# Optimization experiments

Hardware: AMD Instinct MI355X
Metric: run time of the kernel (lower is better)

The kernel has to match this reference:

```python
import jax, jax.numpy as jnp
import numpy as np

B, L, D, DK, DV = 8, 2048, 1024, 1024, 1024

def setup_inputs() -> dict:
    key = jax.random.key(0)
    ks = jax.random.split(key, 8)
    # scale inputs/weights down so exp(scores) is numerically stable
    # (original softmax has no max-subtraction)
    x = jax.random.normal(ks[0], (B, L, D), dtype=jnp.float32) * 0.05
    Wq = jax.random.normal(ks[1], (D, DK), dtype=jnp.float32) * 0.05
    bq = jax.random.normal(ks[2], (DK,), dtype=jnp.float32) * 0.05
    Wk = jax.random.normal(ks[3], (D, DK), dtype=jnp.float32) * 0.05
    bk = jax.random.normal(ks[4], (DK,), dtype=jnp.float32) * 0.05
    Wv = jax.random.normal(ks[5], (D, DV), dtype=jnp.float32) * 0.05
    bv = jax.random.normal(ks[6], (DV,), dtype=jnp.float32) * 0.05
    actulength = jax.random.randint(ks[7], (B,), 1, L, dtype=jnp.int32)
    return {"x": x, "actulength": actulength, "Wq": Wq, "bq": bq,
            "Wk": Wk, "bk": bk, "Wv": Wv, "bv": bv}

def reference(x, actulength, Wq, bq, Wk, bk, Wv, bv):
    # QKV projections
    Q = x @ Wq + bq                      # [B, L, DK]
    K = x @ Wk + bk                      # [B, L, DK]
    V = x @ Wv + bv                      # [B, L, DV]
    scale = 1.0 / jnp.sqrt(jnp.float32(DK))
    scores = jnp.einsum('bld,bmd->blm', Q, K) * scale  # [B, L, L]
    # custom padding-aware softmax: subtract padding count from the sum
    s = jnp.exp(scores)
    tsum = jnp.sum(s, axis=2)            # [B, L]
    padding = (L - actulength).astype(s.dtype)[:, None]  # [B, 1]
    atten = s / (tsum - padding)[:, :, None]
    return jnp.einsum('blm,bmv->blv', atten, V)  # [B, L, DV]
```

## Files before the change

### kernel.cpp

```cpp
#include <hip/hip_runtime.h>
#include <hip/hip_bf16.h>
#include <cstdint>

#define DEV __device__ __forceinline__

typedef __attribute__((ext_vector_type(8))) __bf16 bf16x8;
typedef __attribute__((ext_vector_type(4))) float f32x4;

DEV ushort f2bf(float f){
  uint32_t u = __builtin_bit_cast(uint32_t, f);
  u += 0x7fffu + ((u >> 16) & 1u);
  return (ushort)(u >> 16);
}

DEV void gll16(const void* g, void* l){
  __builtin_amdgcn_global_load_lds((const __attribute__((address_space(1))) void*)g,
                                   (__attribute__((address_space(3))) void*)l, 16, 0, 0);
}

template<int MODE>
__global__ __launch_bounds__(512, 2) void gemm256(
    const ushort* __restrict__ A, const ushort* __restrict__ Bt,
    const float* __restrict__ bias,
    ushort* __restrict__ Cb, float* __restrict__ Cf, ushort* __restrict__ VTout,
    int gm, int gn, int K, int lda, int ldb, int ldc,
    size_t sA, size_t sB, size_t sC,
    float scale, float* __restrict__ partial, const float* __restrict__ denom,
    int Mrows, int nch)
{
  __shared__ __align__(16) ushort As[4][128][64];
  __shared__ __align__(16) ushort Bs[4][128][64];

  const int tid  = threadIdx.x;
  const int lane = tid & 63, wid = tid >> 6;
  const int wm = wid >> 2, wn = wid & 3;
  const int lr = lane & 15, fq = lane >> 4;
  const int lrh = lr >> 1;
  const int lo2 = ((lane & 1) << 2) | fq;

  const int nwg = gridDim.x;
  const int per = nwg >> 3;
  const int id  = blockIdx.x;
  const int swz = (id & 7) * per + (id >> 3);
  const int gmn = gm * gn;
  const int bz  = swz / gmn;
  const int rr  = swz - bz * gmn;
  const int q4  = rr >> 4, w4 = rr & 15;
  const int nsm = gm >> 2;
  const int stm = q4 % nsm, stn = q4 / nsm;
  const int bm  = (stm << 2) + (w4 & 3);
  const int bn  = (stn << 2) + (w4 >> 2);

  const ushort* Ab = A  + (size_t)bz * sA + (size_t)bm * 256 * (size_t)lda;
  const ushort* Bb = Bt + (size_t)bz * sB + (size_t)bn * 256 * (size_t)ldb;
  const int NT = K >> 5;

  auto srcOff = [&](int c, int ld)->size_t{
    int R = c >> 3, ci = c & 7, u = ci ^ (R & 7);
    return (size_t)(2*R + (u >> 2)) * (size_t)(ld*2) + (size_t)((u & 3) << 4);
  };
  const char* srcA0 = (const char*)Ab + srcOff(tid,       lda);
  const char* srcA1 = (const char*)Ab + srcOff(512 + tid, lda);
  const char* srcB0 = (const char*)Bb + srcOff(tid,       ldb);
  const char* srcB1 = (const char*)Bb + srcOff(512 + tid, ldb);
  char* AsB = (char*)As;
  char* BsB = (char*)Bs;
  const int dst0 = (wid << 6) * 16;
  const int dst1 = (512 + (wid << 6)) * 16;

  auto stageA = [&](int t){
    const int sb = (t & 3) << 14;
    const size_t kb = (size_t)t << 6;
    gll16(srcA0 + kb, AsB + sb + dst0);
    gll16(srcA1 + kb, AsB + sb + dst1);
  };
  auto stageB = [&](int t){
    const int sb = (t & 3) << 14;
    const size_t kb = (size_t)t << 6;
    gll16(srcB0 + kb, BsB + sb + dst0);
    gll16(srcB1 + kb, BsB + sb + dst1);
  };

  f32x4 acc[8][4];
  const f32x4 z = {0.f, 0.f, 0.f, 0.f};
#pragma unroll
  for (int m = 0; m < 8; ++m)
#pragma unroll
    for (int n = 0; n < 4; ++n) acc[m][n] = z;

  const int cio  = (lo2 ^ lrh) << 3;
  const int aoff = (wm*64 + lrh)*64 + cio;
  const int boff = (wn*32 + lrh)*64 + cio;

  stageA(0); stageB(0); stageA(1); stageB(1);
  asm volatile("s_waitcnt vmcnt(4)" ::: "memory");
  __builtin_amdgcn_s_barrier();

  for (int t = 0; t < NT; ++t){
    const int s = t & 3;
    const ushort* Asl = (const ushort*)As + (size_t)s*8192;
    const ushort* Bsl = (const ushort*)Bs + (size_t)s*8192;
    const bool pre = (t + 2 < NT);

    bf16x8 bfv[4], af0[4];
#pragma unroll
    for (int n = 0; n < 4; ++n)
      bfv[n] = *(const bf16x8*)&Bsl[boff + n*512];
#pragma unroll
    for (int m = 0; m < 4; ++m)
      af0[m] = *(const bf16x8*)&Asl[aoff + m*512];
    if (pre) stageA(t + 2);
    __builtin_amdgcn_s_barrier();
    __builtin_amdgcn_s_setprio(1);
#pragma unroll
    for (int m = 0; m < 4; ++m)
#pragma unroll
      for (int n = 0; n < 4; ++n)
        acc[m][n] = __builtin_amdgcn_mfma_f32_16x16x32_bf16(af0[m], bfv[n], acc[m][n], 0, 0, 0);
    __builtin_amdgcn_s_setprio(0);
    __builtin_amdgcn_s_barrier();

    bf16x8 af1[4];
#pragma unroll
    for (int m = 0; m < 4; ++m)
      af1[m] = *(const bf16x8*)&Asl[aoff + (m + 4)*512];
    if (pre) stageB(t + 2);
    __builtin_amdgcn_s_barrier();
    __builtin_amdgcn_s_setprio(1);
#pragma unroll
    for (int m = 0; m < 4; ++m)
#pragma unroll
      for (int n = 0; n < 4; ++n)
        acc[m + 4][n] = __builtin_amdgcn_mfma_f32_16x16x32_bf16(af1[m], bfv[n], acc[m + 4][n], 0, 0, 0);
    __builtin_amdgcn_s_setprio(0);

    if (t < NT - 1){
      if (t + 2 < NT) asm volatile("s_waitcnt vmcnt(4)" ::: "memory");
      else            asm volatile("s_waitcnt vmcnt(0)" ::: "memory");
      __builtin_amdgcn_s_barrier();
    }
  }

  const int rbase = bm*256 + wm*128 + fq*4;
  const int cbase = bn*256 + wn*64 + lr;

  if (MODE == 0){
    if (bn >= 8){
#pragma unroll
      for (int m = 0; m < 8; ++m){
        int r0 = rbase + m*16;
        int b = r0 >> 11, l = r0 & 2047;
        ushort* vb = VTout + (size_t)b * 1024 * 2048;
#pragma unroll
        for (int n = 0; n < 4; ++n){
          int c = cbase + n*16;
          float bvv = bias[c];
          ushort4 u4;
          u4.x = f2bf(acc[m][n][0] + bvv);
          u4.y = f2bf(acc[m][n][1] + bvv);
          u4.z = f2bf(acc[m][n][2] + bvv);
          u4.w = f2bf(acc[m][n][3] + bvv);
          *(ushort4*)&vb[(size_t)(c - 2048)*2048 + l] = u4;
        }
      }
    } else {
      ushort* dst = Cb + (size_t)bz * sC;
#pragma unroll
      for (int m = 0; m < 8; ++m){
        int r0 = rbase + m*16;
#pragma unroll
        for (int n = 0; n < 4; ++n){
          int c = cbase + n*16;
          float bvv = bias[c];
#pragma unroll
          for (int i = 0; i < 4; ++i)
            dst[(size_t)(r0 + i)*ldc + c] = f2bf(acc[m][n][i] + bvv);
        }
      }
    }
  } else if (MODE == 1){
    ushort* dst = Cb + (size_t)bz * sC;
#pragma unroll
    for (int m = 0; m < 8; ++m){
      int r0 = rbase + m*16;
#pragma unroll
      for (int i = 0; i < 4; ++i){
        int r = r0 + i;
        float rs = 0.f;
#pragma unroll
        for (int n = 0; n < 4; ++n){
          float v = __expf(acc[m][n][i] * scale);
          dst[(size_t)r*ldc + cbase + n*16] = f2bf(v);
          rs += v;
        }
        rs += __shfl_xor(rs, 1);
        rs += __shfl_xor(rs, 2);
        rs += __shfl_xor(rs, 4);
        rs += __shfl_xor(rs, 8);
        if (lr == 0)
          partial[((size_t)bz*Mrows + r)*nch + (bn*4 + wn)] = rs;
      }
    }
  } else {
    float* dst = Cf + (size_t)bz * sC;
#pragma unroll
    for (int m = 0; m < 8; ++m){
      int r0 = rbase + m*16;
#pragma unroll
      for (int i = 0; i < 4; ++i){
        int r = r0 + i;
        float inv = 1.0f / denom[(size_t)bz*Mrows + r];
#pragma unroll
        for (int n = 0; n < 4; ++n)
          dst[(size_t)r*ldc + cbase + n*16] = acc[m][n][i] * inv;
      }
    }
  }
}


__global__ void denom_k(const float* __restrict__ partial, const int* __restrict__ alen,
                        float* __restrict__ denom, int L, int nch){
  int i = blockIdx.x*blockDim.x + threadIdx.x;
  int b = i / L;
  const float* p = partial + (size_t)i*nch;
  float s = 0.f;
  for (int j = 0; j < nch; j++) s += p[j];
  denom[i] = s - (float)(L - alen[b]);
}

__global__ void cvt_f32_bf16(const float* __restrict__ in, ushort* __restrict__ out, long n4){
  long i = (long)blockIdx.x*blockDim.x + threadIdx.x;
  if (i >= n4) return;
  float4 f = ((const float4*)in)[i];
  ushort4 u;
  u.x = f2bf(f.x); u.y = f2bf(f.y); u.z = f2bf(f.z); u.w = f2bf(f.w);
  ((ushort4*)out)[i] = u;
}

__global__ __launch_bounds__(256) void transpose_f32_bf16(
    const float* __restrict__ in, ushort* __restrict__ out, int R, int C){
  __shared__ ushort t[32][33];
  int tx = threadIdx.x, ty = threadIdx.y;
  int c0 = blockIdx.x*32, r0 = blockIdx.y*32;
#pragma unroll
  for (int i = 0; i < 4; i++)
    t[ty + i*8][tx] = f2bf(in[(size_t)(r0 + ty + i*8)*C + c0 + tx]);
  __syncthreads();
#pragma unroll
  for (int i = 0; i < 4; i++)
    out[(size_t)(c0 + ty + i*8)*R + r0 + tx] = t[tx][ty + i*8];
}

__global__ void pack_bias(const float* __restrict__ q, const float* __restrict__ k,
                          const float* __restrict__ v, float* __restrict__ o){
  int i = blockIdx.x*blockDim.x + threadIdx.x;
  o[i] = (i < 1024) ? q[i] : (i < 2048 ? k[i-1024] : v[i-2048]);
}


extern "C" void kernel_launch(void* const* d_in, const int* in_sizes, int n_in,
                              void* d_out, int out_size, void* d_ws, size_t ws_size,
                              hipStream_t stream){
  const int B = 8, L = 2048, D = 1024, DK = 1024, DV = 1024;
  const float scale = 0.03125f;

  const float* x  = (const float*)d_in[0];
  const int* alen = (const int*)d_in[1];
  const float* Wq = (const float*)d_in[2];
  const float* bq = (const float*)d_in[3];
  const float* Wk = (const float*)d_in[4];
  const float* bk = (const float*)d_in[5];
  const float* Wv = (const float*)d_in[6];
  const float* bv = (const float*)d_in[7];
  float* out = (float*)d_out;

  char* ws = (char*)d_ws;
  size_t off = 0;
  auto alloc = [&](size_t bytes) -> void* {
    void* p = ws + off;
    off += (bytes + 255) & ~(size_t)255;
    return p;
  };
  ushort* xb     = (ushort*)alloc((size_t)B*L*D*2);
  ushort* wqkvT  = (ushort*)alloc((size_t)3*DK*D*2);
  float*  bqkv   = (float*)alloc((size_t)3*DK*4);
  ushort* QK     = (ushort*)alloc((size_t)B*L*2*DK*2);
  ushort* VTb    = (ushort*)alloc((size_t)B*DV*L*2);
  ushort* S      = (ushort*)alloc((size_t)B*L*L*2);
  float* partial = (float*)alloc((size_t)B*L*32*4);
  float* denom   = (float*)alloc((size_t)B*L*4);
  if (off > ws_size) return;

  dim3 tb(32, 8);

  long n4 = (long)B*L*D/4;
  cvt_f32_bf16<<<dim3((unsigned)((n4 + 255)/256)), 256, 0, stream>>>(x, xb, n4);

  transpose_f32_bf16<<<dim3(DK/32, D/32), tb, 0, stream>>>(Wq, wqkvT,          D, DK);
  transpose_f32_bf16<<<dim3(DK/32, D/32), tb, 0, stream>>>(Wk, wqkvT + DK*D,   D, DK);
  transpose_f32_bf16<<<dim3(DV/32, D/32), tb, 0, stream>>>(Wv, wqkvT + 2*DK*D, D, DV);
  pack_bias<<<dim3(12), 256, 0, stream>>>(bq, bk, bv, bqkv);

  gemm256<0><<<dim3(64*12), 512, 0, stream>>>(
      xb, wqkvT, bqkv, QK, nullptr, VTb, 64, 12, D, D, D, 2*DK,
      0, 0, 0, 0.f, nullptr, nullptr, 0, 0);

  gemm256<1><<<dim3(8*8*8), 512, 0, stream>>>(
      QK , QK + DK , nullptr, S, nullptr, nullptr, 8, 8, DK,
      2*DK, 2*DK, L,
      (size_t)L*2*DK, (size_t)L*2*DK, (size_t)L*L, scale, partial, nullptr, L, 32);

  denom_k<<<dim3(B*L/256), 256, 0, stream>>>(partial, alen, denom, L, 32);

  gemm256<2><<<dim3(8*4*8), 512, 0, stream>>>(
      S, VTb, nullptr, nullptr, out, nullptr, 8, 4, L, L, L, DV,
      (size_t)L*L, (size_t)DV*L, (size_t)L*DV, 1.f, nullptr, denom, L, 0);
}
```

Baseline: 299.7 us.

## Shrink GEMM tiles to 256x128 with 4 waves, fuse denom into PV GEMM

The GEMM is reworked from 512 threads and 256x256 tiles with a 4-stage LDS ring into 256 threads and 256x128 tiles with double buffering and a single barrier per k-step. The denominator reduction kernel is folded into the epilogue of the final GEMM, and the three weight transposes are merged into one launch. The goal is more workgroups, lower LDS use per block and fewer kernel launches. The cost is less reuse per tile and a shallower prefetch pipeline, with an unconditional vmcnt(0) wait every iteration.

```diff
diff --git a/kernel.cpp b/kernel.cpp
--- a/kernel.cpp
+++ b/kernel.cpp
@@ -19,21 +19,22 @@
 }
 
 template<int MODE>
-__global__ __launch_bounds__(512, 2) void gemm256(
+__global__ __launch_bounds__(256, 2) void gemm256(
     const ushort* __restrict__ A, const ushort* __restrict__ Bt,
     const float* __restrict__ bias,
     ushort* __restrict__ Cb, float* __restrict__ Cf, ushort* __restrict__ VTout,
     int gm, int gn, int K, int lda, int ldb, int ldc,
     size_t sA, size_t sB, size_t sC,
-    float scale, float* __restrict__ partial, const float* __restrict__ denom,
-    int Mrows, int nch)
+    float scale, float* __restrict__ partial, const int* __restrict__ alen,
+    int Mrows, int Lpad)
 {
-  __shared__ __align__(16) ushort As[4][128][64];
-  __shared__ __align__(16) ushort Bs[4][128][64];
+  __shared__ __align__(16) ushort As[2][128][64];
+  __shared__ __align__(16) ushort Bs[2][64][64];
+  __shared__ float dnls[256];
 
   const int tid  = threadIdx.x;
   const int lane = tid & 63, wid = tid >> 6;
-  const int wm = wid >> 2, wn = wid & 3;
+  const int wm = wid >> 1, wn = wid & 1;
   const int lr = lane & 15, fq = lane >> 4;
   const int lrh = lr >> 1;
   const int lo2 = ((lane & 1) << 2) | fq;
@@ -52,33 +53,32 @@
   const int bn  = (stn << 2) + (w4 >> 2);
 
   const ushort* Ab = A  + (size_t)bz * sA + (size_t)bm * 256 * (size_t)lda;
-  const ushort* Bb = Bt + (size_t)bz * sB + (size_t)bn * 256 * (size_t)ldb;
+  const ushort* Bb = Bt + (size_t)bz * sB + (size_t)bn * 128 * (size_t)ldb;
   const int NT = K >> 5;
 
   auto srcOff = [&](int c, int ld)->size_t{
     int R = c >> 3, ci = c & 7, u = ci ^ (R & 7);
     return (size_t)(2*R + (u >> 2)) * (size_t)(ld*2) + (size_t)((u & 3) << 4);
   };
-  const char* srcA0 = (const char*)Ab + srcOff(tid,       lda);
-  const char* srcA1 = (const char*)Ab + srcOff(512 + tid, lda);
-  const char* srcB0 = (const char*)Bb + srcOff(tid,       ldb);
-  const char* srcB1 = (const char*)Bb + srcOff(512 + tid, ldb);
+  const char* srcA[4]; const char* srcB[2];
+#pragma unroll
+  for (int q = 0; q < 4; ++q) srcA[q] = (const char*)Ab + srcOff(q*256 + tid, lda);
+#pragma unroll
+  for (int q = 0; q < 2; ++q) srcB[q] = (const char*)Bb + srcOff(q*256 + tid, ldb);
   char* AsB = (char*)As;
   char* BsB = (char*)Bs;
-  const int dst0 = (wid << 6) * 16;
-  const int dst1 = (512 + (wid << 6)) * 16;
-
-  auto stageA = [&](int t){
-    const int sb = (t & 3) << 14;
+  const int dstw = (wid << 6) * 16;
+
+  auto stage = [&](int t){
+    const int sa = (t & 1) << 14;
+    const int sb = (t & 1) << 13;
     const size_t kb = (size_t)t << 6;
-    gll16(srcA0 + kb, AsB + sb + dst0);
-    gll16(srcA1 + kb, AsB + sb + dst1);
-  };
-  auto stageB = [&](int t){
-    const int sb = (t & 3) << 14;
-    const size_t kb = (size_t)t << 6;
-    gll16(srcB0 + kb, BsB + sb + dst0);
-    gll16(srcB1 + kb, BsB + sb + dst1);
+#pragma unroll
+    for (int q = 0; q < 4; ++q)
+      gll16(srcA[q] + kb, AsB + sa + q*4096 + dstw);
+#pragma unroll
+    for (int q = 0; q < 2; ++q)
+      gll16(srcB[q] + kb, BsB + sb + q*4096 + dstw);
   };
 
   f32x4 acc[8][4];
@@ -92,60 +92,44 @@
   const int aoff = (wm*64 + lrh)*64 + cio;
   const int boff = (wn*32 + lrh)*64 + cio;
 
-  stageA(0); stageB(0); stageA(1); stageB(1);
-  asm volatile("s_waitcnt vmcnt(4)" ::: "memory");
+  stage(0);
+  asm volatile("s_waitcnt vmcnt(0)" ::: "memory");
   __builtin_amdgcn_s_barrier();
 
   for (int t = 0; t < NT; ++t){
-    const int s = t & 3;
+    const int s = t & 1;
     const ushort* Asl = (const ushort*)As + (size_t)s*8192;
-    const ushort* Bsl = (const ushort*)Bs + (size_t)s*8192;
-    const bool pre = (t + 2 < NT);
-
-    bf16x8 bfv[4], af0[4];
+    const ushort* Bsl = (const ushort*)Bs + (size_t)s*4096;
+
+    if (t + 1 < NT) stage(t + 1);
+
+    bf16x8 bfv[4], af[8];
 #pragma unroll
     for (int n = 0; n < 4; ++n)
       bfv[n] = *(const bf16x8*)&Bsl[boff + n*512];
 #pragma unroll
-    for (int m = 0; m < 4; ++m)
-      af0[m] = *(const bf16x8*)&Asl[aoff + m*512];
-    if (pre) stageA(t + 2);
-    __builtin_amdgcn_s_barrier();
+    for (int m = 0; m < 8; ++m)
+      af[m] = *(const bf16x8*)&Asl[aoff + m*512];
+
     __builtin_amdgcn_s_setprio(1);
 #pragma unroll
-    for (int m = 0; m < 4; ++m)
+    for (int m = 0; m < 8; ++m)
 #pragma unroll
       for (int n = 0; n < 4; ++n)
-        acc[m][n] = __builtin_amdgcn_mfma_f32_16x16x32_bf16(af0[m], bfv[n], acc[m][n], 0, 0, 0);
+        acc[m][n] = __builtin_amdgcn_mfma_f32_16x16x32_bf16(af[m], bfv[n], acc[m][n], 0, 0, 0);
     __builtin_amdgcn_s_setprio(0);
-    __builtin_amdgcn_s_barrier();
-
-    bf16x8 af1[4];
-#pragma unroll
-    for (int m = 0; m < 4; ++m)
-      af1[m] = *(const bf16x8*)&Asl[aoff + (m + 4)*512];
-    if (pre) stageB(t + 2);
-    __builtin_amdgcn_s_barrier();
-    __builtin_amdgcn_s_setprio(1);
-#pragma unroll
-    for (int m = 0; m < 4; ++m)
-#pragma unroll
-      for (int n = 0; n < 4; ++n)
-        acc[m + 4][n] = __builtin_amdgcn_mfma_f32_16x16x32_bf16(af1[m], bfv[n], acc[m + 4][n], 0, 0, 0);
-    __builtin_amdgcn_s_setprio(0);
-
-    if (t < NT - 1){
-      if (t + 2 < NT) asm volatile("s_waitcnt vmcnt(4)" ::: "memory");
-      else            asm volatile("s_waitcnt vmcnt(0)" ::: "memory");
+
+    if (t + 1 < NT){
+      asm volatile("s_waitcnt vmcnt(0)" ::: "memory");
       __builtin_amdgcn_s_barrier();
     }
   }
 
   const int rbase = bm*256 + wm*128 + fq*4;
-  const int cbase = bn*256 + wn*64 + lr;
+  const int cbase = bn*128 + wn*64 + lr;
 
   if (MODE == 0){
-    if (bn >= 8){
+    if (bn >= 16){
 #pragma unroll
       for (int m = 0; m < 8; ++m){
         int r0 = rbase + m*16;
@@ -198,10 +182,19 @@
         rs += __shfl_xor(rs, 4);
         rs += __shfl_xor(rs, 8);
         if (lr == 0)
-          partial[((size_t)bz*Mrows + r)*nch + (bn*4 + wn)] = rs;
+          partial[((size_t)bz*Mrows + r)*32 + (bn*2 + wn)] = rs;
       }
     }
   } else {
+    {
+      int r = bm*256 + tid;
+      const float* p = partial + ((size_t)bz*Mrows + r)*32;
+      float ssum = 0.f;
+#pragma unroll
+      for (int j = 0; j < 32; ++j) ssum += p[j];
+      dnls[tid] = ssum - (float)(Lpad - alen[bz]);
+    }
+    __syncthreads();
     float* dst = Cf + (size_t)bz * sC;
 #pragma unroll
     for (int m = 0; m < 8; ++m){
@@ -209,7 +202,7 @@
 #pragma unroll
       for (int i = 0; i < 4; ++i){
         int r = r0 + i;
-        float inv = 1.0f / denom[(size_t)bz*Mrows + r];
+        float inv = 1.0f / dnls[r - bm*256];
 #pragma unroll
         for (int n = 0; n < 4; ++n)
           dst[(size_t)r*ldc + cbase + n*16] = acc[m][n][i] * inv;
@@ -218,16 +211,6 @@
   }
 }
 
-
-__global__ void denom_k(const float* __restrict__ partial, const int* __restrict__ alen,
-                        float* __restrict__ denom, int L, int nch){
-  int i = blockIdx.x*blockDim.x + threadIdx.x;
-  int b = i / L;
-  const float* p = partial + (size_t)i*nch;
-  float s = 0.f;
-  for (int j = 0; j < nch; j++) s += p[j];
-  denom[i] = s - (float)(L - alen[b]);
-}
 
 __global__ void cvt_f32_bf16(const float* __restrict__ in, ushort* __restrict__ out, long n4){
   long i = (long)blockIdx.x*blockDim.x + threadIdx.x;
@@ -238,9 +221,13 @@
   ((ushort4*)out)[i] = u;
 }
 
-__global__ __launch_bounds__(256) void transpose_f32_bf16(
-    const float* __restrict__ in, ushort* __restrict__ out, int R, int C){
+__global__ __launch_bounds__(256) void transpose_w3(
+    const float* __restrict__ Wq, const float* __restrict__ Wk,
+    const float* __restrict__ Wv, ushort* __restrict__ out, int R, int C){
   __shared__ ushort t[32][33];
+  int zz = blockIdx.z;
+  const float* in = (zz == 0) ? Wq : (zz == 1 ? Wk : Wv);
+  ushort* o = out + (size_t)zz * R * C;
   int tx = threadIdx.x, ty = threadIdx.y;
   int c0 = blockIdx.x*32, r0 = blockIdx.y*32;
 #pragma unroll
@@ -249,7 +236,7 @@
   __syncthreads();
 #pragma unroll
   for (int i = 0; i < 4; i++)
-    out[(size_t)(c0 + ty + i*8)*R + r0 + tx] = t[tx][ty + i*8];
+    o[(size_t)(c0 + ty + i*8)*R + r0 + tx] = t[tx][ty + i*8];
 }
 
 __global__ void pack_bias(const float* __restrict__ q, const float* __restrict__ k,
@@ -289,31 +276,24 @@
   ushort* VTb    = (ushort*)alloc((size_t)B*DV*L*2);
   ushort* S      = (ushort*)alloc((size_t)B*L*L*2);
   float* partial = (float*)alloc((size_t)B*L*32*4);
-  float* denom   = (float*)alloc((size_t)B*L*4);
   if (off > ws_size) return;
-
-  dim3 tb(32, 8);
 
   long n4 = (long)B*L*D/4;
   cvt_f32_bf16<<<dim3((unsigned)((n4 + 255)/256)), 256, 0, stream>>>(x, xb, n4);
 
-  transpose_f32_bf16<<<dim3(DK/32, D/32), tb, 0, stream>>>(Wq, wqkvT,          D, DK);
-  transpose_f32_bf16<<<dim3(DK/32, D/32), tb, 0, stream>>>(Wk, wqkvT + DK*D,   D, DK);
-  transpose_f32_bf16<<<dim3(DV/32, D/32), tb, 0, stream>>>(Wv, wqkvT + 2*DK*D, D, DV);
+  transpose_w3<<<dim3(DK/32, D/32, 3), dim3(32, 8), 0, stream>>>(Wq, Wk, Wv, wqkvT, D, DK);
   pack_bias<<<dim3(12), 256, 0, stream>>>(bq, bk, bv, bqkv);
 
-  gemm256<0><<<dim3(64*12), 512, 0, stream>>>(
-      xb, wqkvT, bqkv, QK, nullptr, VTb, 64, 12, D, D, D, 2*DK,
+  gemm256<0><<<dim3(64*24), 256, 0, stream>>>(
+      xb, wqkvT, bqkv, QK, nullptr, VTb, 64, 24, D, D, D, 2*DK,
       0, 0, 0, 0.f, nullptr, nullptr, 0, 0);
 
-  gemm256<1><<<dim3(8*8*8), 512, 0, stream>>>(
-      QK , QK + DK , nullptr, S, nullptr, nullptr, 8, 8, DK,
+  gemm256<1><<<dim3(8*16*8), 256, 0, stream>>>(
+      QK , QK + DK , nullptr, S, nullptr, nullptr, 8, 16, DK,
       2*DK, 2*DK, L,
-      (size_t)L*2*DK, (size_t)L*2*DK, (size_t)L*L, scale, partial, nullptr, L, 32);
-
-  denom_k<<<dim3(B*L/256), 256, 0, stream>>>(partial, alen, denom, L, 32);
-
-  gemm256<2><<<dim3(8*4*8), 512, 0, stream>>>(
-      S, VTb, nullptr, nullptr, out, nullptr, 8, 4, L, L, L, DV,
-      (size_t)L*L, (size_t)DV*L, (size_t)L*DV, 1.f, nullptr, denom, L, 0);
-}
+      (size_t)L*2*DK, (size_t)L*2*DK, (size_t)L*L, scale, partial, nullptr, L, 0);
+
+  gemm256<2><<<dim3(8*8*8), 256, 0, stream>>>(
+      S, VTb, nullptr, nullptr, out, nullptr, 8, 8, L, L, L, DV,
+      (size_t)L*L, (size_t)DV*L, (size_t)L*DV, 1.f, partial, alen, L, L);
+}
```

After: 315.5 us. +5.3%, slower.
